# Kernel optimization log

Measured on AMD Instinct MI355X. Metric: run time of the kernel, lower is better.

The kernel has to match this reference:

```python
import jax, jax.numpy as jnp
import numpy as np
from math import log

B, L, D = 2, 4096, 2048
H, Dh, C, KW = 16, 128, 64, 4
EPS = 1e-5
SCALE = 0.02


def setup_inputs() -> dict:
    key = jax.random.key(0)
    ks = jax.random.split(key, 16)
    rn = lambda k, shp, sc=SCALE: jax.random.normal(k, shp, jnp.float32) * sc
    # dt_bias built like the torch module
    dt = jnp.exp(jax.random.uniform(ks[7], (H,)) * (log(0.1) - log(0.001)) + log(0.001))
    dt = jnp.clip(dt, 0.0001, None)
    dt_bias = dt + jnp.log(-jnp.expm1(-dt))
    return {
        "x": jax.random.normal(ks[0], (B, L, D), jnp.float32),
        "Wq": rn(ks[1], (H * Dh, D)),
        "Wk": rn(ks[2], (H * Dh, D)),
        "Wv": rn(ks[3], (H * Dh, D)),
        "Wb": rn(ks[4], (H, D)),
        "Wa": rn(ks[5], (H, D)),
        "A_log": jnp.log(jax.random.uniform(ks[6], (H,), minval=0.01, maxval=16.0)),
        "dt_bias": dt_bias,
        "conv_q": rn(ks[8], (H * Dh, 1, KW), 0.2),
        "conv_k": rn(ks[9], (H * Dh, 1, KW), 0.2),
        "conv_v": rn(ks[10], (H * Dh, 1, KW), 0.2),
        "Wg": rn(ks[11], (H * Dh, D)),
        "norm_w": jnp.ones((Dh,), jnp.float32),
        "Wo": rn(ks[12], (D, H * Dh)),
        "S0": jnp.zeros((B, H, Dh, Dh), jnp.float32),
    }


def _causal_dwconv(x, w):
    # x: [B,L,Ch]; w: [Ch,1,KW] depthwise causal conv (left pad KW-1), then SiLU
    y = jax.lax.conv_general_dilated(
        x.transpose(0, 2, 1), w, (1,), [(KW - 1, 0)],
        feature_group_count=w.shape[0], dimension_numbers=("NCH", "OIH", "NCH"))
    return jax.nn.silu(y).transpose(0, 2, 1)


def reference(x, Wq, Wk, Wv, Wb, Wa, A_log, dt_bias, conv_q, conv_k, conv_v, Wg, norm_w, Wo, S0):
    q = _causal_dwconv(x @ Wq.T, conv_q).reshape(B, L, H, Dh).transpose(0, 2, 1, 3)  # [B,H,L,Dh]
    k = _causal_dwconv(x @ Wk.T, conv_k).reshape(B, L, H, Dh).transpose(0, 2, 1, 3)
    v = _causal_dwconv(x @ Wv.T, conv_v).reshape(B, L, H, Dh).transpose(0, 2, 1, 3)
    beta = jax.nn.sigmoid(x @ Wb.T).transpose(0, 2, 1)                                # [B,H,L]
    g = (-jnp.exp(A_log) * jax.nn.softplus(x @ Wa.T + dt_bias)).transpose(0, 2, 1)    # [B,H,L]
    l2 = lambda t: t / jnp.maximum(jnp.linalg.norm(t, axis=-1, keepdims=True), 1e-12)
    q = l2(q) / (Dh ** 0.5)
    k = l2(k)

    N = L // C  # chunks (L divisible by C)
    chop = lambda t: jnp.moveaxis(t.reshape(B, H, N, C, Dh), 2, 0)   # [N,B,H,C,Dh]
    qc, kc, vc = chop(q), chop(k), chop(v)
    betac = jnp.moveaxis(beta.reshape(B, H, N, C), 2, 0)[..., None]  # [N,B,H,C,1]
    gc = jnp.moveaxis(g.reshape(B, H, N, C), 2, 0)                   # [N,B,H,C]

    eye = jnp.eye(C, dtype=x.dtype)
    m_incl = jnp.tril(jnp.ones((C, C), bool))
    m_strict = jnp.tril(jnp.ones((C, C), bool), -1)

    def step(S, ch):
        Q, Kc, V, bet, gch = ch
        lg = jnp.cumsum(gch, axis=-1)          # log gamma, [B,H,C]
        gamma = jnp.exp(lg)
        lgC = lg[..., -1:]
        gCr = jnp.exp(lgC - lg)
        gammaC = jnp.exp(lgC)[..., None]       # [B,H,1,1]
        Qd = Q * gamma[..., None]
        Kd = gCr[..., None] * Kc
        Sd = S * gammaC
        Gam = lg[..., :, None] - lg[..., None, :]
        ratio = jnp.exp(jnp.where(m_strict, Gam, -jnp.inf))
        A = eye + bet * ratio * (Kc @ jnp.swapaxes(Kc, -1, -2))
        T = jax.scipy.linalg.solve_triangular(A, jnp.broadcast_to(eye, A.shape), lower=True)
        Wm = T @ (bet * gamma[..., None] * Kc)
        U = T @ (bet * V)
        St = jnp.swapaxes(S, -1, -2)
        GM = jnp.exp(jnp.where(m_incl, Gam, -jnp.inf))
        mid = U - Wm @ St                      # [B,H,C,Dh]
        O = Qd @ St + ((Q @ jnp.swapaxes(Kc, -1, -2)) * GM) @ mid
        S_new = Sd + jnp.swapaxes(mid, -1, -2) @ Kd
        return S_new, O

    S_fin, Os = jax.lax.scan(step, S0, (qc, kc, vc, betac, gc))
    o = Os.transpose(1, 0, 3, 2, 4).reshape(B, L, H, Dh)  # chunks -> [B,L,H,Dh]
    gate = (x @ Wg.T).reshape(B, L, H, Dh)
    # gated RMSNorm: rms-normalize o, scale by weight, gate with SiLU(g)
    o = o * jax.lax.rsqrt(jnp.mean(o * o, axis=-1, keepdims=True) + EPS) * norm_w * jax.nn.silu(gate)
    return (o.reshape(B, L, H * Dh) @ Wo.T, S_fin)
```

## Files before the change

kernel.cpp:

```cpp
#include <hip/hip_runtime.h>
#include <math.h>

#define B_   2
#define L_   4096
#define D_   2048
#define H_   16
#define DH   128
#define CH   64
#define NCH  64
#define HD   2048
#define BH   32
#define BHL  131072
#define PSZ  16777216ull

typedef unsigned short u16;
typedef __attribute__((ext_vector_type(8))) short bf16x8;
typedef __attribute__((ext_vector_type(4))) float f32x4;
#define MFMA16(a, b, c) __builtin_amdgcn_mfma_f32_16x16x32_bf16(a, b, c, 0, 0, 0)

static __device__ __forceinline__ float sigm(float x) { return 1.0f / (1.0f + expf(-x)); }

static __device__ __forceinline__ float b2f(u16 u) {
    union { float f; unsigned int i; } v; v.i = ((unsigned int)u) << 16; return v.f;
}
static __device__ __forceinline__ u16 f2b(float f) {
    union { float f; unsigned int i; } v; v.f = f;
    unsigned int r = v.i + 0x7fffu + ((v.i >> 16) & 1u);
    return (u16)(r >> 16);
}
static __device__ __forceinline__ void b8ld(const u16* p, float* d) {
    uint4 u = *(const uint4*)p;
    d[0] = b2f((u16)(u.x & 0xffff)); d[1] = b2f((u16)(u.x >> 16));
    d[2] = b2f((u16)(u.y & 0xffff)); d[3] = b2f((u16)(u.y >> 16));
    d[4] = b2f((u16)(u.z & 0xffff)); d[5] = b2f((u16)(u.z >> 16));
    d[6] = b2f((u16)(u.w & 0xffff)); d[7] = b2f((u16)(u.w >> 16));
}
static __device__ __forceinline__ void b8st(const float* s, u16* p) {
    uint4 u;
    u.x = (unsigned)f2b(s[0]) | ((unsigned)f2b(s[1]) << 16);
    u.y = (unsigned)f2b(s[2]) | ((unsigned)f2b(s[3]) << 16);
    u.z = (unsigned)f2b(s[4]) | ((unsigned)f2b(s[5]) << 16);
    u.w = (unsigned)f2b(s[6]) | ((unsigned)f2b(s[7]) << 16);
    *(uint4*)p = u;
}
static __device__ __forceinline__ void cstore(float* p, float v) { *p = v; }
static __device__ __forceinline__ void cstore(u16* p, float v) { *p = f2b(v); }

static __device__ __forceinline__ void async16(const u16* g, u16* l) {
    __builtin_amdgcn_global_load_lds(
        (const __attribute__((address_space(1))) unsigned int*)g,
        (__attribute__((address_space(3))) unsigned int*)l, 16, 0, 0);
}

static __device__ __forceinline__ void bar_lgkm() {
    asm volatile("s_waitcnt lgkmcnt(0)" ::: "memory");
    __builtin_amdgcn_sched_barrier(0);
    __builtin_amdgcn_s_barrier();
    __builtin_amdgcn_sched_barrier(0);
}
static __device__ __forceinline__ void wait_vm0() {
    asm volatile("s_waitcnt vmcnt(0)" ::: "memory");
    __builtin_amdgcn_sched_barrier(0);
}

__global__ __launch_bounds__(256) void cvt_f2b(const float* __restrict__ in,
                                               u16* __restrict__ out, int n8) {
    int i = blockIdx.x * 256 + threadIdx.x;
    if (i >= n8) return;
    float t[8];
    float4 a = *(const float4*)(in + (size_t)i * 8);
    float4 b = *(const float4*)(in + (size_t)i * 8 + 4);
    t[0] = a.x; t[1] = a.y; t[2] = a.z; t[3] = a.w;
    t[4] = b.x; t[5] = b.y; t[6] = b.z; t[7] = b.w;
    b8st(t, out + (size_t)i * 8);
}

template <typename TC>
__global__ __launch_bounds__(512) void gemm_bt_async(const u16* __restrict__ A,
                                                     const u16* __restrict__ Bm,
                                                     TC* __restrict__ Cm,
                                                     int M, int N, int K) {
    __shared__ __align__(16) u16 sA[2][256 * 64];
    __shared__ __align__(16) u16 sB[2][256 * 64];
    const int tid = threadIdx.x;
    const int w = tid >> 6, lane = tid & 63, lq = lane >> 4, ln = lane & 15;
    const int wm = w >> 2, wn = w & 3;
    const int nx = gridDim.x;
    const int lin = blockIdx.y * nx + blockIdx.x;
    const int chunk = (nx * gridDim.y) >> 3;
    const int wg = (lin & 7) * chunk + (lin >> 3);
    const int mbase = (wg / nx) * 256, nbase = (wg % nx) * 256;

    f32x4 acc[8][4];
#pragma unroll
    for (int mt = 0; mt < 8; mt++)
#pragma unroll
        for (int nt = 0; nt < 4; nt++) acc[mt][nt] = (f32x4){0.f, 0.f, 0.f, 0.f};

    auto stage = [&](int kt, int p) {
        const int k0 = kt * 64;
#pragma unroll
        for (int j = 0; j < 4; j++) {
            int c = tid + 512 * j;
            int row = c >> 3;
            int oct = (c & 7) ^ (row & 7);
            async16(A + (size_t)(mbase + row) * K + k0 + oct * 8, &sA[p][c * 8]);
            async16(Bm + (size_t)(nbase + row) * K + k0 + oct * 8, &sB[p][c * 8]);
        }
    };

    const int NT = K >> 6;
    stage(0, 0);
    wait_vm0();
    __builtin_amdgcn_s_barrier();
    __builtin_amdgcn_sched_barrier(0);

    for (int t = 0; t < NT; t++) {
        const int p = t & 1;
        if (t + 1 < NT) stage(t + 1, p ^ 1);
        __builtin_amdgcn_s_setprio(1);
#pragma unroll
        for (int ks = 0; ks < 2; ks++) {
            const int o = ks * 4 + lq;
            bf16x8 bfr[4];
#pragma unroll
            for (int nt = 0; nt < 4; nt++) {
                int nn = wn * 64 + nt * 16 + ln;
                bfr[nt] = *(const bf16x8*)&sB[p][(nn << 6) + ((o ^ (nn & 7)) << 3)];
            }
#pragma unroll
            for (int mt = 0; mt < 8; mt++) {
                int m = wm * 128 + mt * 16 + ln;
                bf16x8 af = *(const bf16x8*)&sA[p][(m << 6) + ((o ^ (m & 7)) << 3)];
#pragma unroll
                for (int nt = 0; nt < 4; nt++)
                    acc[mt][nt] = MFMA16(af, bfr[nt], acc[mt][nt]);
            }
        }
        __builtin_amdgcn_s_setprio(0);
        if (t + 1 < NT) {
            wait_vm0();
            bar_lgkm();
        }
    }
#pragma unroll
    for (int mt = 0; mt < 8; mt++)
#pragma unroll
        for (int nt = 0; nt < 4; nt++) {
            int col = nbase + wn * 64 + nt * 16 + ln;
#pragma unroll
            for (int r = 0; r < 4; r++) {
                int row = mbase + wm * 128 + mt * 16 + lq * 4 + r;
                cstore(Cm + (size_t)row * N + col, acc[mt][nt][r]);
            }
        }
}

__global__ __launch_bounds__(256) void conv_silu_norm(const u16* __restrict__ pre,
                                                      const float* __restrict__ w,
                                                      u16* __restrict__ out, int mode) {
    int wid = blockIdx.x * 4 + (threadIdx.x >> 6);
    int lane = threadIdx.x & 63;
    int l = wid & (L_ - 1);
    int bh = wid >> 12;
    int b = bh >> 4, h = bh & 15;

    float vals[2];
    float sumsq = 0.0f;
#pragma unroll
    for (int s = 0; s < 2; s++) {
        int d = lane + 64 * s;
        int c = h * DH + d;
        const u16* col = pre + (size_t)b * L_ * HD + c;
        float acc = 0.0f;
        if (l >= 3) {
            acc = w[c * 4 + 0] * b2f(col[(size_t)(l - 3) * HD]) +
                  w[c * 4 + 1] * b2f(col[(size_t)(l - 2) * HD]) +
                  w[c * 4 + 2] * b2f(col[(size_t)(l - 1) * HD]) +
                  w[c * 4 + 3] * b2f(col[(size_t)l * HD]);
        } else {
#pragma unroll
            for (int j = 0; j < 4; j++) {
                int ll = l - 3 + j;
                if (ll >= 0) acc += w[c * 4 + j] * b2f(col[(size_t)ll * HD]);
            }
        }
        float y = acc * sigm(acc);
        vals[s] = y;
        sumsq += y * y;
    }
    if (mode < 2) {
#pragma unroll
        for (int m = 32; m >= 1; m >>= 1) sumsq += __shfl_xor(sumsq, m, 64);
        float scale = 1.0f / fmaxf(sqrtf(sumsq), 1e-12f);
        if (mode == 0) scale *= 0.08838834764831843f;
        vals[0] *= scale;
        vals[1] *= scale;
    }
    u16* o = out + ((size_t)bh * L_ + l) * DH;
    o[lane] = f2b(vals[0]);
    o[lane + 64] = f2b(vals[1]);
}

__global__ __launch_bounds__(64) void proj_small(const float* __restrict__ x,
                                                 const float* __restrict__ Wb,
                                                 const float* __restrict__ Wa,
                                                 float* __restrict__ bpre,
                                                 float* __restrict__ apre) {
    int row = blockIdx.x;
    int lane = threadIdx.x;
    const float* xr = x + (size_t)row * D_;
    float xv[32];
#pragma unroll
    for (int j = 0; j < 32; j++) xv[j] = xr[lane + 64 * j];
    for (int h = 0; h < 16; h++) {
        const float* wr = Wb + (size_t)h * D_;
        float acc = 0.0f;
#pragma unroll
        for (int j = 0; j < 32; j++) acc += xv[j] * wr[lane + 64 * j];
#pragma unroll
        for (int m = 32; m >= 1; m >>= 1) acc += __shfl_xor(acc, m, 64);
        if (lane == 0) bpre[(size_t)row * 16 + h] = acc;
    }
    for (int h = 0; h < 16; h++) {
        const float* wr = Wa + (size_t)h * D_;
        float acc = 0.0f;
#pragma unroll
        for (int j = 0; j < 32; j++) acc += xv[j] * wr[lane + 64 * j];
#pragma unroll
        for (int m = 32; m >= 1; m >>= 1) acc += __shfl_xor(acc, m, 64);
        if (lane == 0) apre[(size_t)row * 16 + h] = acc;
    }
}

__global__ __launch_bounds__(256) void beta_g_k(const float* __restrict__ bpre,
                                                const float* __restrict__ apre,
                                                const float* __restrict__ A_log,
                                                const float* __restrict__ dt_bias,
                                                float* __restrict__ beta, float* __restrict__ g) {
    int gi = blockIdx.x * 256 + threadIdx.x;
    int l = gi & (L_ - 1);
    int bh = gi >> 12;
    int b = bh >> 4, h = bh & 15;
    float bp = bpre[((size_t)b * L_ + l) * 16 + h];
    float ap = apre[((size_t)b * L_ + l) * 16 + h] + dt_bias[h];
    float sp = (ap > 20.0f) ? ap : log1pf(expf(ap));
    beta[(size_t)bh * L_ + l] = 1.0f / (1.0f + expf(-bp));
    g[(size_t)bh * L_ + l] = -expf(A_log[h]) * sp;
}

__global__ __launch_bounds__(256) void prep_chunks(u16* __restrict__ q, u16* __restrict__ k,
                                                   u16* __restrict__ v,
                                                   const float* __restrict__ beta,
                                                   const float* __restrict__ g,
                                                   u16* __restrict__ Wm, u16* __restrict__ W2,
                                                   float* __restrict__ gamC) {
    __shared__ __align__(16) u16 sKb[64 * 136];
    __shared__ __align__(16) float sA[64 * 65];
    __shared__ __align__(16) float sT[64 * 68];
    __shared__ __align__(16) u16 sKsT[128 * 64];
    __shared__ float sLg[CH], sGam[CH], sGcr[CH], sBeta[CH];

    u16* sVsT = (u16*)sA;
    u16* sThi = (u16*)sT;
    u16* sTlo = (u16*)sT + 4096;

    const int cid = blockIdx.x;
    const int bh = cid >> 6, n = cid & 63;
    const int tid = threadIdx.x;
    const int w = tid >> 6, lane = tid & 63, lq = lane >> 4, ln = lane & 15;
    const size_t cbase = ((size_t)bh * L_ + (size_t)n * CH) * DH;
    u16* qw = q + cbase;
    u16* kw = k + cbase;
    u16* vc = v + cbase;

    bf16x8 aQ[4];
    {
        const u16* qrow = qw + (size_t)(w * 16 + ln) * DH;
#pragma unroll
        for (int ks = 0; ks < 4; ks++)
            aQ[ks] = *(const bf16x8*)(qrow + ks * 32 + lq * 8);
    }
#pragma unroll
    for (int rep = 0; rep < 4; rep++) {
        int f = tid + 256 * rep;
        int row = f >> 4, c8 = (f & 15) * 8;
        *(uint4*)&sKb[row * 136 + c8] = *(const uint4*)(kw + (size_t)row * DH + c8);
    }
    if (tid < 64) {
        float lg = g[(size_t)bh * L_ + (size_t)n * CH + tid];
#pragma unroll
        for (int off = 1; off < 64; off <<= 1) {
            float u = __shfl_up(lg, off, 64);
            if (tid >= off) lg += u;
        }
        float lgC = __shfl(lg, 63, 64);
        sLg[tid] = lg;
        sGam[tid] = expf(lg);
        sGcr[tid] = expf(lgC - lg);
        sBeta[tid] = beta[(size_t)bh * L_ + (size_t)n * CH + tid];
        if (tid == 63) gamC[cid] = expf(lgC);
    }
    __syncthreads();

    {
        f32x4 accA[4], accQ[4];
#pragma unroll
        for (int nt = 0; nt < 4; nt++) {
            accA[nt] = (f32x4){0.f, 0.f, 0.f, 0.f};
            accQ[nt] = (f32x4){0.f, 0.f, 0.f, 0.f};
        }
#pragma unroll
        for (int ks = 0; ks < 4; ks++) {
            int k0 = ks * 32 + lq * 8;
            bf16x8 aK = *(const bf16x8*)&sKb[(w * 16 + ln) * 136 + k0];
#pragma unroll
            for (int nt = 0; nt < 4; nt++) {
                bf16x8 bK = *(const bf16x8*)&sKb[(nt * 16 + ln) * 136 + k0];
                accA[nt] = MFMA16(aK, bK, accA[nt]);
                accQ[nt] = MFMA16(aQ[ks], bK, accQ[nt]);
            }
        }
        for (int idx = tid; idx < 64 * 68; idx += 256) sT[idx] = 0.f;
        u16* w2c = W2 + (size_t)cid * CH * CH;
#pragma unroll
        for (int nt = 0; nt < 4; nt++) {
            int j = nt * 16 + ln;
            float lgj = sLg[j];
#pragma unroll
            for (int r = 0; r < 4; r++) {
                int i = w * 16 + lq * 4 + r;
                float dexp = expf(fminf(sLg[i] - lgj, 0.f));
                sA[i * 65 + j] = (j < i) ? sBeta[i] * dexp * accA[nt][r] : 0.f;
                w2c[i * CH + j] = f2b((j <= i) ? accQ[nt][r] * dexp : 0.f);
            }
        }
    }
    __syncthreads();

    float colv[16];
    {
        const int i0 = w * 16;
        colv[0] = (ln == 0) ? 1.f : 0.f;
#pragma unroll
        for (int i = 1; i < 16; i++) {
            float acc = (ln == i) ? 1.f : 0.f;
#pragma unroll
            for (int kk = 0; kk < 15; kk++) {
                if (kk < i) acc -= sA[(i0 + i) * 65 + i0 + kk] * colv[kk];
            }
            colv[i] = acc;
        }
    }
#pragma unroll
    for (int rep = 0; rep < 4; rep++) {
        int f = tid + 256 * rep;
        int i = f >> 4, d8 = (f & 15) * 8;
        float tq[8];
        b8ld(qw + (size_t)i * DH + d8, tq);
        float sq = sGam[i];
#pragma unroll
        for (int jj = 0; jj < 8; jj++) tq[jj] *= sq;
        b8st(tq, qw + (size_t)i * DH + d8);
    }
    {
        int e = tid >> 1, qh = tid & 1;
#pragma unroll
        for (int oo = 0; oo < 4; oo++) {
            int i0 = qh * 32 + oo * 8;
            u16 op[8];
#pragma unroll
            for (int jj = 0; jj < 8; jj++)
                op[jj] = f2b(b2f(sKb[(i0 + jj) * 136 + e]) * sGcr[i0 + jj]);
            int slot = ((i0 >> 3) ^ (e & 7));
            uint4 pk;
            pk.x = (unsigned)op[0] | ((unsigned)op[1] << 16);
            pk.y = (unsigned)op[2] | ((unsigned)op[3] << 16);
            pk.z = (unsigned)op[4] | ((unsigned)op[5] << 16);
            pk.w = (unsigned)op[6] | ((unsigned)op[7] << 16);
            *(uint4*)(kw + e * 64 + slot * 8) = pk;
        }
    }
    if (lq == 0) {
#pragma unroll
        for (int i = 0; i < 16; i++) sT[(w * 16 + i) * 68 + w * 16 + ln] = colv[i];
    }
    __syncthreads();

    auto trijob = [&](int bi, int bj) {
        float accv[4] = {0.f, 0.f, 0.f, 0.f};
        for (int kb = bj; kb < bi; kb++) {
#pragma unroll
            for (int kk = 0; kk < 16; kk++) {
                float bv = sT[(kb * 16 + kk) * 68 + bj * 16 + ln];
#pragma unroll
                for (int r = 0; r < 4; r++)
                    accv[r] += sA[(bi * 16 + lq * 4 + r) * 65 + kb * 16 + kk] * bv;
            }
        }
        float xv[4] = {0.f, 0.f, 0.f, 0.f};
#pragma unroll
        for (int kk = 0; kk < 16; kk++) {
            float bv = __shfl(accv[kk & 3], (kk >> 2) * 16 + ln, 64);
#pragma unroll
            for (int r = 0; r < 4; r++)
                xv[r] -= sT[(bi * 16 + lq * 4 + r) * 68 + bi * 16 + kk] * bv;
        }
#pragma unroll
        for (int r = 0; r < 4; r++)
            sT[(bi * 16 + lq * 4 + r) * 68 + bj * 16 + ln] = xv[r];
    };
    if (w < 3) trijob(w + 1, w);
    __syncthreads();
    if (w < 2) trijob(w + 2, w);
    __syncthreads();
    if (w == 0) trijob(3, 0);
    __syncthreads();

    {
        int e = tid >> 1, qh = tid & 1;
#pragma unroll
        for (int oo = 0; oo < 4; oo++) {
            int i0 = qh * 32 + oo * 8;
            u16 op[8];
#pragma unroll
            for (int jj = 0; jj < 8; jj++) {
                int kkw = i0 + jj;
                op[jj] = f2b(b2f(sKb[kkw * 136 + e]) * (sBeta[kkw] * sGam[kkw]));
            }
            int slot = ((i0 >> 3) ^ (e & 7));
            uint4 pk;
            pk.x = (unsigned)op[0] | ((unsigned)op[1] << 16);
            pk.y = (unsigned)op[2] | ((unsigned)op[3] << 16);
            pk.z = (unsigned)op[4] | ((unsigned)op[5] << 16);
            pk.w = (unsigned)op[6] | ((unsigned)op[7] << 16);
            *(uint4*)&sKsT[e * 64 + slot * 8] = pk;
        }
    }
    float tvs[16];
    {
        int ti = tid >> 2, kks = (tid & 3) * 16;
#pragma unroll
        for (int j = 0; j < 16; j++) tvs[j] = sT[ti * 68 + kks + j];
    }
    __syncthreads();

    {
        int ti = tid >> 2, kks = (tid & 3) * 16;
#pragma unroll
        for (int h = 0; h < 2; h++) {
            u16 hi8[8], lo8[8];
#pragma unroll
            for (int j = 0; j < 8; j++) {
                float tv = tvs[h * 8 + j];
                u16 hb = f2b(tv);
                hi8[j] = hb;
                lo8[j] = f2b(tv - b2f(hb));
            }
            int io = (kks >> 3) + h;
            int slot = io ^ (ti & 7);
            uint4 ph, pl;
            ph.x = (unsigned)hi8[0] | ((unsigned)hi8[1] << 16);
            ph.y = (unsigned)hi8[2] | ((unsigned)hi8[3] << 16);
            ph.z = (unsigned)hi8[4] | ((unsigned)hi8[5] << 16);
            ph.w = (unsigned)hi8[6] | ((unsigned)hi8[7] << 16);
            pl.x = (unsigned)lo8[0] | ((unsigned)lo8[1] << 16);
            pl.y = (unsigned)lo8[2] | ((unsigned)lo8[3] << 16);
            pl.z = (unsigned)lo8[4] | ((unsigned)lo8[5] << 16);
            pl.w = (unsigned)lo8[6] | ((unsigned)lo8[7] << 16);
            *(uint4*)&sThi[ti * 64 + slot * 8] = ph;
            *(uint4*)&sTlo[ti * 64 + slot * 8] = pl;
        }
    }
#pragma unroll
    for (int rep = 0; rep < 4; rep++) {
        int f = tid + 256 * rep;
        int row = f >> 4, c8 = (f & 15) * 8;
        *(uint4*)&sKb[row * 136 + c8] = *(const uint4*)(vc + (size_t)row * DH + c8);
    }
    __syncthreads();

    {
        int e = tid >> 1, qh = tid & 1;
#pragma unroll
        for (int oo = 0; oo < 4; oo++) {
            int i0 = qh * 32 + oo * 8;
            u16 op[8];
#pragma unroll
            for (int jj = 0; jj < 8; jj++) {
                int kkw = i0 + jj;
                op[jj] = f2b(b2f(sKb[kkw * 136 + e]) * sBeta[kkw]);
            }
            int slot = ((i0 >> 3) ^ (e & 7));
            uint4 pk;
            pk.x = (unsigned)op[0] | ((unsigned)op[1] << 16);
            pk.y = (unsigned)op[2] | ((unsigned)op[3] << 16);
            pk.z = (unsigned)op[4] | ((unsigned)op[5] << 16);
            pk.w = (unsigned)op[6] | ((unsigned)op[7] << 16);
            *(uint4*)&sVsT[e * 64 + slot * 8] = pk;
        }
    }
    __syncthreads();

    {
        u16* wmc = Wm + (size_t)cid * CH * DH;
        bf16x8 bK[2][2], bV[2][2];
#pragma unroll
        for (int et = 0; et < 2; et++) {
            int eb = w * 32 + et * 16 + ln;
#pragma unroll
            for (int ks = 0; ks < 2; ks++) {
                int o = ks * 4 + lq;
                bK[et][ks] = *(const bf16x8*)&sKsT[eb * 64 + ((o ^ (eb & 7)) << 3)];
                bV[et][ks] = *(const bf16x8*)&sVsT[eb * 64 + ((o ^ (eb & 7)) << 3)];
            }
        }
#pragma unroll
        for (int it = 0; it < 4; it++) {
            int ia = it * 16 + ln;
            bf16x8 ahi[2], alo[2];
#pragma unroll
            for (int ks = 0; ks < 2; ks++) {
                int o = ks * 4 + lq;
                ahi[ks] = *(const bf16x8*)&sThi[ia * 64 + ((o ^ (ia & 7)) << 3)];
                alo[ks] = *(const bf16x8*)&sTlo[ia * 64 + ((o ^ (ia & 7)) << 3)];
            }
#pragma unroll
            for (int et = 0; et < 2; et++) {
                f32x4 aK = (f32x4){0.f, 0.f, 0.f, 0.f};
                f32x4 aV = (f32x4){0.f, 0.f, 0.f, 0.f};
#pragma unroll
                for (int ks = 0; ks < 2; ks++) {
                    aK = MFMA16(ahi[ks], bK[et][ks], aK);
                    aK = MFMA16(alo[ks], bK[et][ks], aK);
                    aV = MFMA16(ahi[ks], bV[et][ks], aV);
                    aV = MFMA16(alo[ks], bV[et][ks], aV);
                }
                int ecol = w * 32 + et * 16 + ln;
#pragma unroll
                for (int r = 0; r < 4; r++) {
                    int irow = it * 16 + lq * 4 + r;
                    wmc[(size_t)irow * DH + ecol] = f2b(aK[r]);
                    vc[(size_t)irow * DH + ecol] = f2b(aV[r]);
                }
            }
        }
    }
}

__global__ __launch_bounds__(256) void scan_mfma(const u16* __restrict__ Wm,
                                                 const u16* __restrict__ U,
                                                 const u16* __restrict__ Qd,
                                                 const u16* __restrict__ Kd,
                                                 const u16* __restrict__ W2,
                                                 const float* __restrict__ gamC,
                                                 const float* __restrict__ S0,
                                                 float* __restrict__ Og,
                                                 float* __restrict__ Sfin) {
    __shared__ __align__(16) u16 sWm[2][64 * 128];
    __shared__ __align__(16) u16 sQd[2][64 * 128];
    __shared__ __align__(16) u16 sW2[2][64 * 64];
    __shared__ __align__(16) u16 sKdT[2][128 * 64];
    __shared__ __align__(16) u16 sS[2][16 * 136];
    __shared__ __align__(16) u16 sMidT[16 * 72];

    const int bid = blockIdx.x;
    const int xcd = bid & 7, slot = bid >> 3;
    const int bh = xcd + 8 * (slot >> 3), dg = slot & 7, d0 = dg * 16;
    const int tid = threadIdx.x;
    const int w = tid >> 6, lane = tid & 63, lq = lane >> 4, ln = lane & 15;

    f32x4 S_t[2];
#pragma unroll
    for (int t2 = 0; t2 < 2; t2++)
#pragma unroll
        for (int r = 0; r < 4; r++)
            S_t[t2][r] = S0[(size_t)bh * DH * DH + (size_t)(d0 + lq * 4 + r) * DH + w * 32 + t2 * 16 + ln];

    auto stage_async = [&](int m, int p) {
        const size_t cid2 = (size_t)bh * NCH + m;
        const u16* wmc = Wm + cid2 * CH * DH;
        const size_t tb = ((size_t)bh * L_ + (size_t)m * CH) * DH;
        const u16* qc  = Qd + tb;
        const u16* kc  = Kd + tb;
        const u16* w2c = W2 + cid2 * CH * CH;
#pragma unroll
        for (int j = 0; j < 4; j++) {
            int c = tid + 256 * j;
            int row = c >> 4;
            int osrc = (c & 15) ^ (row & 7);
            async16(wmc + (size_t)row * DH + osrc * 8, &sWm[p][c * 8]);
            async16(qc  + (size_t)row * DH + osrc * 8, &sQd[p][c * 8]);
            async16(kc + (size_t)c * 8, &sKdT[p][c * 8]);
        }
#pragma unroll
        for (int j = 0; j < 2; j++) {
            int c = tid + 256 * j;
            int row = c >> 3;
            int osrc = (c & 7) ^ (row & 7);
            async16(w2c + (size_t)row * CH + osrc * 8, &sW2[p][c * 8]);
        }
    };
    auto write_ss = [&](int p) {
#pragma unroll
        for (int t2 = 0; t2 < 2; t2++)
#pragma unroll
            for (int r = 0; r < 4; r++)
                sS[p][(lq * 4 + r) * 136 + w * 32 + t2 * 16 + ln] = f2b(S_t[t2][r]);
    };

    u16 ureg[4], uregN[4];
    auto load_ureg = [&](int m, u16* dst) {
        const u16* uc = U + ((size_t)bh * L_ + (size_t)m * CH) * DH;
#pragma unroll
        for (int r = 0; r < 4; r++)
            dst[r] = uc[(size_t)(w * 16 + lq * 4 + r) * DH + d0 + ln];
    };

    stage_async(0, 0);
    load_ureg(0, ureg);
    float gCur = gamC[(size_t)bh * NCH];
    float gNext = 0.f;
    write_ss(0);
    wait_vm0();
    bar_lgkm();

    for (int n = 0; n < NCH; n++) {
        const int p = n & 1;
        const bool hasN = (n + 1 < NCH);
        if (hasN) {
            stage_async(n + 1, p ^ 1);
            load_ureg(n + 1, uregN);
            gNext = gamC[(size_t)bh * NCH + n + 1];
        }

        {
            f32x4 macc = (f32x4){0.f, 0.f, 0.f, 0.f};
            const int i = w * 16 + ln;
#pragma unroll
            for (int ks = 0; ks < 4; ks++) {
                int o = ks * 4 + lq;
                bf16x8 a = *(const bf16x8*)&sWm[p][i * 128 + ((o ^ (i & 7)) << 3)];
                bf16x8 b = *(const bf16x8*)&sS[p][ln * 136 + ks * 32 + lq * 8];
                macc = MFMA16(a, b, macc);
            }
#pragma unroll
            for (int r = 0; r < 4; r++) {
                int ii = w * 16 + lq * 4 + r;
                float mv = b2f(ureg[r]) - macc[r];
                sMidT[ln * 72 + ii] = f2b(mv);
            }
        }
        bar_lgkm();

        {
            f32x4 oacc = (f32x4){0.f, 0.f, 0.f, 0.f};
            const int i = w * 16 + ln;
#pragma unroll
            for (int ks = 0; ks < 4; ks++) {
                int o = ks * 4 + lq;
                bf16x8 a = *(const bf16x8*)&sQd[p][i * 128 + ((o ^ (i & 7)) << 3)];
                bf16x8 b = *(const bf16x8*)&sS[p][ln * 136 + ks * 32 + lq * 8];
                oacc = MFMA16(a, b, oacc);
            }
#pragma unroll
            for (int ks = 0; ks < 2; ks++) {
                int o = ks * 4 + lq;
                bf16x8 a = *(const bf16x8*)&sW2[p][i * 64 + ((o ^ (i & 7)) << 3)];
                bf16x8 b = *(const bf16x8*)&sMidT[ln * 72 + ks * 32 + lq * 8];
                oacc = MFMA16(a, b, oacc);
            }
#pragma unroll
            for (int r = 0; r < 4; r++) {
                int ii = w * 16 + lq * 4 + r;
                Og[((size_t)bh * L_ + (size_t)n * CH + ii) * DH + d0 + ln] = oacc[r];
            }
        }

#pragma unroll
        for (int t2 = 0; t2 < 2; t2++)
#pragma unroll
            for (int r = 0; r < 4; r++) S_t[t2][r] *= gCur;
#pragma unroll
        for (int ks = 0; ks < 2; ks++) {
            bf16x8 a = *(const bf16x8*)&sMidT[ln * 72 + ks * 32 + lq * 8];
#pragma unroll
            for (int t2 = 0; t2 < 2; t2++) {
                int e = (2 * w + t2) * 16 + ln;
                int o = ks * 4 + lq;
                bf16x8 b = *(const bf16x8*)&sKdT[p][e * 64 + ((o ^ (e & 7)) << 3)];
                S_t[t2] = MFMA16(a, b, S_t[t2]);
            }
        }

        if (hasN) {
            write_ss(p ^ 1);
#pragma unroll
            for (int r = 0; r < 4; r++) ureg[r] = uregN[r];
            gCur = gNext;
            wait_vm0();
            bar_lgkm();
        }
    }

#pragma unroll
    for (int t2 = 0; t2 < 2; t2++)
#pragma unroll
        for (int r = 0; r < 4; r++)
            Sfin[(size_t)bh * DH * DH + (size_t)(d0 + lq * 4 + r) * DH + w * 32 + t2 * 16 + ln] = S_t[t2][r];
}

__global__ __launch_bounds__(256) void epilogue_gate(const float* __restrict__ Ob,
                                                     const u16* __restrict__ gpre,
                                                     const float* __restrict__ norm_w,
                                                     u16* __restrict__ gated) {
    int wid = blockIdx.x * 4 + (threadIdx.x >> 6);
    int lane = threadIdx.x & 63;
    int l = wid & (L_ - 1);
    int bh = wid >> 12;
    int b = bh >> 4, h = bh & 15;
    const float* orow = Ob + ((size_t)bh * L_ + l) * DH;
    float o0 = orow[lane], o1 = orow[lane + 64];
    float ss = o0 * o0 + o1 * o1;
#pragma unroll
    for (int m = 32; m >= 1; m >>= 1) ss += __shfl_xor(ss, m, 64);
    float r = rsqrtf(ss * (1.0f / 128.0f) + 1e-5f);
    size_t gidx = ((size_t)b * L_ + l) * HD + h * DH;
    float gp0 = b2f(gpre[gidx + lane]), gp1 = b2f(gpre[gidx + lane + 64]);
    gated[gidx + lane] = f2b(o0 * r * norm_w[lane] * (gp0 * sigm(gp0)));
    gated[gidx + lane + 64] = f2b(o1 * r * norm_w[lane + 64] * (gp1 * sigm(gp1)));
}

extern "C" void kernel_launch(void* const* d_in, const int* in_sizes, int n_in,
                              void* d_out, int out_size, void* d_ws, size_t ws_size,
                              hipStream_t stream) {
    const float* x       = (const float*)d_in[0];
    const float* Wq      = (const float*)d_in[1];
    const float* Wk      = (const float*)d_in[2];
    const float* Wv      = (const float*)d_in[3];
    const float* Wb      = (const float*)d_in[4];
    const float* Wa      = (const float*)d_in[5];
    const float* A_log   = (const float*)d_in[6];
    const float* dt_bias = (const float*)d_in[7];
    const float* conv_q  = (const float*)d_in[8];
    const float* conv_k  = (const float*)d_in[9];
    const float* conv_v  = (const float*)d_in[10];
    const float* Wg      = (const float*)d_in[11];
    const float* norm_w  = (const float*)d_in[12];
    const float* Wo      = (const float*)d_in[13];
    const float* S0      = (const float*)d_in[14];
    float* out = (float*)d_out;

    u16* Pb = (u16*)d_ws;
    u16* Qb = Pb + PSZ;
    u16* Kb = Qb + PSZ;
    u16* Vb = Kb + PSZ;
    u16* W2b = Vb + PSZ;
    u16* xb  = W2b + PSZ / 2;
    u16* wbuf = xb + PSZ;
    float* bpre = (float*)(wbuf + 4194304);
    float* apre = bpre + BHL;
    float* betab = apre + BHL;
    float* gbuf = betab + BHL;
    float* gamC = gbuf + BHL;

    float* Obuf = out;
    float* Sfin = out + PSZ;

    dim3 gblk(8, 32);
    const int W8 = 2048 * 2048 / 8;

    cvt_f2b<<<8192, 256, 0, stream>>>(x, xb, (int)(PSZ / 8));
    cvt_f2b<<<2048, 256, 0, stream>>>(Wq, wbuf, W8);
    gemm_bt_async<u16><<<gblk, 512, 0, stream>>>(xb, wbuf, Pb, 8192, 2048, 2048);
    conv_silu_norm<<<32768, 256, 0, stream>>>(Pb, conv_q, Qb, 0);
    cvt_f2b<<<2048, 256, 0, stream>>>(Wk, wbuf, W8);
    gemm_bt_async<u16><<<gblk, 512, 0, stream>>>(xb, wbuf, Pb, 8192, 2048, 2048);
    conv_silu_norm<<<32768, 256, 0, stream>>>(Pb, conv_k, Kb, 1);
    cvt_f2b<<<2048, 256, 0, stream>>>(Wv, wbuf, W8);
    gemm_bt_async<u16><<<gblk, 512, 0, stream>>>(xb, wbuf, Pb, 8192, 2048, 2048);
    conv_silu_norm<<<32768, 256, 0, stream>>>(Pb, conv_v, Vb, 2);
    proj_small<<<8192, 64, 0, stream>>>(x, Wb, Wa, bpre, apre);
    beta_g_k<<<512, 256, 0, stream>>>(bpre, apre, A_log, dt_bias, betab, gbuf);
    prep_chunks<<<2048, 256, 0, stream>>>(Qb, Kb, Vb, betab, gbuf, Pb, W2b, gamC);
    scan_mfma<<<256, 256, 0, stream>>>(Pb, Vb, Qb, Kb, W2b, gamC, S0, Obuf, Sfin);
    cvt_f2b<<<2048, 256, 0, stream>>>(Wg, wbuf, W8);
    gemm_bt_async<u16><<<gblk, 512, 0, stream>>>(xb, wbuf, Vb, 8192, 2048, 2048);
    epilogue_gate<<<32768, 256, 0, stream>>>(Obuf, Vb, norm_w, Kb);
    cvt_f2b<<<2048, 256, 0, stream>>>(Wo, wbuf, W8);
    gemm_bt_async<float><<<gblk, 512, 0, stream>>>(Kb, wbuf, out, 8192, 2048, 2048);
}
```

Measured before the change: 966.5 us.

## Merge two state-column groups per scan block to share staged chunk tiles

The chunked delta-rule scan now uses 512-thread blocks. Each block covers two 16-row slices of the state, one per group of four waves, so the grid halves from 256 to 128 blocks. The Wm, Qd, Kd and W2 chunk tiles staged in shared memory are now loaded once and shared by both slices, cutting redundant global-to-LDS traffic. The cost is half as many blocks on a GPU with many compute units, and more waves must join each block-wide barrier.

```diff
diff --git a/kernel.cpp b/kernel.cpp
--- a/kernel.cpp
+++ b/kernel.cpp
@@ -548,7 +548,7 @@
     }
 }
 
-__global__ __launch_bounds__(256) void scan_mfma(const u16* __restrict__ Wm,
+__global__ __launch_bounds__(512) void scan_mfma(const u16* __restrict__ Wm,
                                                  const u16* __restrict__ U,
                                                  const u16* __restrict__ Qd,
                                                  const u16* __restrict__ Kd,
@@ -561,21 +561,23 @@
     __shared__ __align__(16) u16 sQd[2][64 * 128];
     __shared__ __align__(16) u16 sW2[2][64 * 64];
     __shared__ __align__(16) u16 sKdT[2][128 * 64];
-    __shared__ __align__(16) u16 sS[2][16 * 136];
-    __shared__ __align__(16) u16 sMidT[16 * 72];
+    __shared__ __align__(16) u16 sS[2][2][16 * 136];
+    __shared__ __align__(16) u16 sMidT[2][16 * 72];
 
     const int bid = blockIdx.x;
     const int xcd = bid & 7, slot = bid >> 3;
-    const int bh = xcd + 8 * (slot >> 3), dg = slot & 7, d0 = dg * 16;
+    const int bh = xcd + 8 * (slot >> 2);
     const int tid = threadIdx.x;
     const int w = tid >> 6, lane = tid & 63, lq = lane >> 4, ln = lane & 15;
+    const int dgrp = w >> 2, wp = w & 3;
+    const int d0 = (slot & 3) * 32 + dgrp * 16;
 
     f32x4 S_t[2];
 #pragma unroll
     for (int t2 = 0; t2 < 2; t2++)
 #pragma unroll
         for (int r = 0; r < 4; r++)
-            S_t[t2][r] = S0[(size_t)bh * DH * DH + (size_t)(d0 + lq * 4 + r) * DH + w * 32 + t2 * 16 + ln];
+            S_t[t2][r] = S0[(size_t)bh * DH * DH + (size_t)(d0 + lq * 4 + r) * DH + wp * 32 + t2 * 16 + ln];
 
     auto stage_async = [&](int m, int p) {
         const size_t cid2 = (size_t)bh * NCH + m;
@@ -585,17 +587,16 @@
         const u16* kc  = Kd + tb;
         const u16* w2c = W2 + cid2 * CH * CH;
 #pragma unroll
-        for (int j = 0; j < 4; j++) {
-            int c = tid + 256 * j;
+        for (int j = 0; j < 2; j++) {
+            int c = tid + 512 * j;
             int row = c >> 4;
             int osrc = (c & 15) ^ (row & 7);
             async16(wmc + (size_t)row * DH + osrc * 8, &sWm[p][c * 8]);
             async16(qc  + (size_t)row * DH + osrc * 8, &sQd[p][c * 8]);
             async16(kc + (size_t)c * 8, &sKdT[p][c * 8]);
         }
-#pragma unroll
-        for (int j = 0; j < 2; j++) {
-            int c = tid + 256 * j;
+        {
+            int c = tid;
             int row = c >> 3;
             int osrc = (c & 7) ^ (row & 7);
             async16(w2c + (size_t)row * CH + osrc * 8, &sW2[p][c * 8]);
@@ -606,7 +607,7 @@
         for (int t2 = 0; t2 < 2; t2++)
 #pragma unroll
             for (int r = 0; r < 4; r++)
-                sS[p][(lq * 4 + r) * 136 + w * 32 + t2 * 16 + ln] = f2b(S_t[t2][r]);
+                sS[dgrp][p][(lq * 4 + r) * 136 + wp * 32 + t2 * 16 + ln] = f2b(S_t[t2][r]);
     };
 
     u16 ureg[4], uregN[4];
@@ -614,7 +615,7 @@
         const u16* uc = U + ((size_t)bh * L_ + (size_t)m * CH) * DH;
 #pragma unroll
         for (int r = 0; r < 4; r++)
-            dst[r] = uc[(size_t)(w * 16 + lq * 4 + r) * DH + d0 + ln];
+            dst[r] = uc[(size_t)(wp * 16 + lq * 4 + r) * DH + d0 + ln];
     };
 
     stage_async(0, 0);
@@ -636,43 +637,43 @@
 
         {
             f32x4 macc = (f32x4){0.f, 0.f, 0.f, 0.f};
-            const int i = w * 16 + ln;
+            const int i = wp * 16 + ln;
 #pragma unroll
             for (int ks = 0; ks < 4; ks++) {
                 int o = ks * 4 + lq;
                 bf16x8 a = *(const bf16x8*)&sWm[p][i * 128 + ((o ^ (i & 7)) << 3)];
-                bf16x8 b = *(const bf16x8*)&sS[p][ln * 136 + ks * 32 + lq * 8];
+                bf16x8 b = *(const bf16x8*)&sS[dgrp][p][ln * 136 + ks * 32 + lq * 8];
                 macc = MFMA16(a, b, macc);
             }
 #pragma unroll
             for (int r = 0; r < 4; r++) {
-                int ii = w * 16 + lq * 4 + r;
+                int ii = wp * 16 + lq * 4 + r;
                 float mv = b2f(ureg[r]) - macc[r];
-                sMidT[ln * 72 + ii] = f2b(mv);
+                sMidT[dgrp][ln * 72 + ii] = f2b(mv);
             }
         }
         bar_lgkm();
 
         {
             f32x4 oacc = (f32x4){0.f, 0.f, 0.f, 0.f};
-            const int i = w * 16 + ln;
+            const int i = wp * 16 + ln;
 #pragma unroll
             for (int ks = 0; ks < 4; ks++) {
                 int o = ks * 4 + lq;
                 bf16x8 a = *(const bf16x8*)&sQd[p][i * 128 + ((o ^ (i & 7)) << 3)];
-                bf16x8 b = *(const bf16x8*)&sS[p][ln * 136 + ks * 32 + lq * 8];
+                bf16x8 b = *(const bf16x8*)&sS[dgrp][p][ln * 136 + ks * 32 + lq * 8];
                 oacc = MFMA16(a, b, oacc);
             }
 #pragma unroll
             for (int ks = 0; ks < 2; ks++) {
                 int o = ks * 4 + lq;
                 bf16x8 a = *(const bf16x8*)&sW2[p][i * 64 + ((o ^ (i & 7)) << 3)];
-                bf16x8 b = *(const bf16x8*)&sMidT[ln * 72 + ks * 32 + lq * 8];
+                bf16x8 b = *(const bf16x8*)&sMidT[dgrp][ln * 72 + ks * 32 + lq * 8];
                 oacc = MFMA16(a, b, oacc);
             }
 #pragma unroll
             for (int r = 0; r < 4; r++) {
-                int ii = w * 16 + lq * 4 + r;
+                int ii = wp * 16 + lq * 4 + r;
                 Og[((size_t)bh * L_ + (size_t)n * CH + ii) * DH + d0 + ln] = oacc[r];
             }
         }
@@ -683,10 +684,10 @@
             for (int r = 0; r < 4; r++) S_t[t2][r] *= gCur;
 #pragma unroll
         for (int ks = 0; ks < 2; ks++) {
-            bf16x8 a = *(const bf16x8*)&sMidT[ln * 72 + ks * 32 + lq * 8];
+            bf16x8 a = *(const bf16x8*)&sMidT[dgrp][ln * 72 + ks * 32 + lq * 8];
 #pragma unroll
             for (int t2 = 0; t2 < 2; t2++) {
-                int e = (2 * w + t2) * 16 + ln;
+                int e = (2 * wp + t2) * 16 + ln;
                 int o = ks * 4 + lq;
                 bf16x8 b = *(const bf16x8*)&sKdT[p][e * 64 + ((o ^ (e & 7)) << 3)];
                 S_t[t2] = MFMA16(a, b, S_t[t2]);
@@ -707,7 +708,7 @@
     for (int t2 = 0; t2 < 2; t2++)
 #pragma unroll
         for (int r = 0; r < 4; r++)
-            Sfin[(size_t)bh * DH * DH + (size_t)(d0 + lq * 4 + r) * DH + w * 32 + t2 * 16 + ln] = S_t[t2][r];
+            Sfin[(size_t)bh * DH * DH + (size_t)(d0 + lq * 4 + r) * DH + wp * 32 + t2 * 16 + ln] = S_t[t2][r];
 }
 
 __global__ __launch_bounds__(256) void epilogue_gate(const float* __restrict__ Ob,
@@ -783,7 +784,7 @@
     proj_small<<<8192, 64, 0, stream>>>(x, Wb, Wa, bpre, apre);
     beta_g_k<<<512, 256, 0, stream>>>(bpre, apre, A_log, dt_bias, betab, gbuf);
     prep_chunks<<<2048, 256, 0, stream>>>(Qb, Kb, Vb, betab, gbuf, Pb, W2b, gamC);
-    scan_mfma<<<256, 256, 0, stream>>>(Pb, Vb, Qb, Kb, W2b, gamC, S0, Obuf, Sfin);
+    scan_mfma<<<128, 512, 0, stream>>>(Pb, Vb, Qb, Kb, W2b, gamC, S0, Obuf, Sfin);
     cvt_f2b<<<2048, 256, 0, stream>>>(Wg, wbuf, W8);
     gemm_bt_async<u16><<<gblk, 512, 0, stream>>>(xb, wbuf, Vb, 8192, 2048, 2048);
     epilogue_gate<<<32768, 256, 0, stream>>>(Obuf, Vb, norm_w, Kb);
```

After: 980.5 us. Within noise of the previous version (+1.4%).
